# Optimization experiments

Hardware: AMD Instinct MI355X
Metric: run time of the kernel (lower is better)

Reference implementation:

```python
import jax, jax.numpy as jnp
import numpy as np

NUM_CHANNEL = 2                      # channels per telescope group
K = 7                                # hexagonal kernel size
N_LEV = [2048, 512, 128, 32, 8]      # pixels per level (stride-2 hex pooling ~ /4)
CHS = [2, 64, 128, 256, 512]         # channel progression n1->n_features->n2->n3->n4


def _iconv(x, idx, w, b):
    # x: [B,C,Nin], idx: [K,Nout], w: [O,C,K] -> [B,O,Nout]
    g = x[:, :, idx]                              # gather neighbours [B,C,K,Nout]
    return jnp.einsum('bckn,ock->bon', g, w) + b[None, :, None]


def _ipool(x, idx):
    # IndexedMaxPool2d: gather then max over kernel positions
    return x[:, :, idx].max(axis=2)               # [B,C,Nout]


def _bn(x, gamma, beta, eps=1e-5):
    # train-mode BatchNorm1d over (batch, pixel) dims, biased variance (torch semantics)
    m = x.mean(axis=(0, 2), keepdims=True)
    v = x.var(axis=(0, 2), keepdims=True)
    return (x - m) / jnp.sqrt(v + eps) * gamma[None, :, None] + beta[None, :, None]


def setup_inputs() -> dict:
    key = jax.random.key(0)
    ks = jax.random.split(key, 40)
    ki = iter(range(40))
    nk = lambda: ks[next(ki)]
    B = 256
    inp = {"x": jax.random.normal(nk(), (B, 2 * NUM_CHANNEL, N_LEV[0]), jnp.float32)}
    for i in range(4):
        inp[f"idx_conv{i+1}"] = jax.random.randint(nk(), (K, N_LEV[i]), 0, N_LEV[i])
        inp[f"idx_pool{i+1}"] = jax.random.randint(nk(), (K, N_LEV[i + 1]), 0, N_LEV[i])
        fan = float(CHS[i] * K)
        inp[f"w{i+1}"] = jax.random.normal(nk(), (CHS[i + 1], CHS[i], K), jnp.float32) / np.float32(np.sqrt(fan))
        inp[f"b{i+1}"] = jnp.zeros((CHS[i + 1],), jnp.float32)
        inp[f"gamma{i+1}"] = jnp.ones((CHS[i + 1],), jnp.float32)
        inp[f"beta{i+1}"] = jnp.zeros((CHS[i + 1],), jnp.float32)
    F = N_LEV[4] * CHS[4]            # 8 * 512 = 4096
    H = F // 2                       # 2048
    inp["lin1_w"] = jax.random.normal(nk(), (H, F), jnp.float32) / np.float32(np.sqrt(F))
    inp["lin1_b"] = jnp.zeros((H,), jnp.float32)
    inp["gamma5"] = jnp.ones((H,), jnp.float32)
    inp["beta5"] = jnp.zeros((H,), jnp.float32)
    inp["lin2_w"] = jax.random.normal(nk(), (3, H), jnp.float32) / np.float32(np.sqrt(H))
    inp["lin2_b"] = jnp.zeros((3,), jnp.float32)
    return inp


def reference(x, idx_conv1, idx_pool1, idx_conv2, idx_pool2, idx_conv3, idx_pool3,
              idx_conv4, idx_pool4, w1, b1, gamma1, beta1, w2, b2, gamma2, beta2,
              w3, b3, gamma3, beta3, w4, b4, gamma4, beta4,
              lin1_w, lin1_b, gamma5, beta5, lin2_w, lin2_b):
    layers = [(idx_conv1, idx_pool1, w1, b1, gamma1, beta1),
              (idx_conv2, idx_pool2, w2, b2, gamma2, beta2),
              (idx_conv3, idx_pool3, w3, b3, gamma3, beta3),
              (idx_conv4, idx_pool4, w4, b4, gamma4, beta4)]
    T = x.shape[1] // NUM_CHANNEL    # number of telescope groups (static)
    outs = []
    for i in range(T):
        o = x[:, i * NUM_CHANNEL:(i + 1) * NUM_CHANNEL, :]
        for (ic, ip, w, b, g, be) in layers:
            # conv -> pool -> bn -> relu (dropout with p=0 is identity)
            o = jax.nn.relu(_bn(_ipool(_iconv(o, ic, w, b), ip), g, be))
        outs.append(o)
    o = jnp.stack(outs, 1).mean(axis=1)          # [B, 512, 8]
    o = o.reshape(o.shape[0], -1)                # [B, 4096]
    o = o @ lin1_w.T + lin1_b                    # [B, 2048]
    m = o.mean(axis=0)
    v = o.var(axis=0)
    o = (o - m) / jnp.sqrt(v + 1e-5) * gamma5 + beta5
    o = jax.nn.relu(o)
    o = o @ lin2_w.T + lin2_b                    # [B, 3]
    cls = jax.nn.log_softmax(o[:, :2], axis=1)   # targets: class=2 (log-softmax), energy=1 (raw)
    return jnp.concatenate([cls, o[:, 2:3]], axis=1)
```

## Files before the change

kernel.cpp:

```cpp
#include <hip/hip_runtime.h>
#include <math.h>

#define B 256
#define KW 7

typedef __bf16 bf16x8 __attribute__((ext_vector_type(8)));
typedef __bf16 bf16x4 __attribute__((ext_vector_type(4)));
typedef float  f32x4  __attribute__((ext_vector_type(4)));

__device__ __forceinline__ void block_reduce2(float& s, float& s2, float* lds) {
    for (int off = 32; off > 0; off >>= 1) {
        s  += __shfl_down(s,  off, 64);
        s2 += __shfl_down(s2, off, 64);
    }
    int wave = threadIdx.x >> 6;
    int lane = threadIdx.x & 63;
    if (lane == 0) { lds[wave * 2] = s; lds[wave * 2 + 1] = s2; }
    __syncthreads();
    if (threadIdx.x == 0) {
        s  = lds[0] + lds[2] + lds[4] + lds[6];
        s2 = lds[1] + lds[3] + lds[5] + lds[7];
    }
}

__global__ __launch_bounds__(256) void k_transpose(const float* __restrict__ x,
                                                   float* __restrict__ A0) {
    int bid = blockIdx.x;
    int nt  = bid & 63;
    int rem = bid >> 6;
    int ci  = rem & 1;
    int t   = rem >> 1;
    int n0  = nt * 32;
    __shared__ float lds[32][257];
    int tid = threadIdx.x;
    int nl  = tid & 31;
    int bq  = tid >> 5;
    int ch  = t * 2 + ci;
    for (int p = 0; p < 32; p++) {
        int b = bq + p * 8;
        lds[nl][b] = x[((size_t)b * 4 + ch) * 2048 + n0 + nl];
    }
    __syncthreads();
    for (int nl2 = 0; nl2 < 32; nl2++) {
        A0[(((size_t)t * 2048 + n0 + nl2) * 2 + ci) * B + tid] = lds[nl2][tid];
    }
}

__global__ __launch_bounds__(256) void k_convpool1(
    const float* __restrict__ act,
    float* __restrict__ P1,
    const float* __restrict__ w,
    const float* __restrict__ bias,
    const int* __restrict__ idx_conv,
    const int* __restrict__ idx_pool,
    float* __restrict__ part1c)
{
    const int Kt = 14, C_out = 64, N_in = 2048, N_out = 512;
    int bid   = blockIdx.x;
    int cot   = bid & 1;
    int colid = bid >> 1;
    int t     = colid / N_out;
    int np    = colid - t * N_out;
    int co0   = cot << 5;

    __shared__ float lds_g[14 * 256];
    __shared__ float lds_w[14 * 33];
    __shared__ int   lds_idx[KW];

    int tid = threadIdx.x;
    int cog = tid >> 6;
    int bl  = tid & 63;

    float pmax[8][4];
    #pragma unroll
    for (int i = 0; i < 8; i++)
        #pragma unroll
        for (int j = 0; j < 4; j++) pmax[i][j] = -INFINITY;

    const float* actT = act + (size_t)t * N_in * 2 * B;

    for (int kp = 0; kp < KW; kp++) {
        int nc = idx_pool[kp * N_out + np];
        if (tid < KW) lds_idx[tid] = idx_conv[tid * N_in + nc];

        float acc[8][4];
        #pragma unroll
        for (int i = 0; i < 8; i++)
            #pragma unroll
            for (int j = 0; j < 4; j++) acc[i][j] = 0.f;

        __syncthreads();
        for (int e = tid; e < 32 * Kt; e += 256) {
            int kk = e % Kt;
            int co = e / Kt;
            lds_w[kk * 33 + co] = w[(size_t)(co0 + co) * Kt + kk];
        }
        for (int r = 0; r < Kt; r++) {
            int ci  = r / KW;
            int k   = r - ci * KW;
            int col = lds_idx[k];
            lds_g[r * 256 + tid] = actT[((size_t)col * 2 + ci) * B + tid];
        }
        __syncthreads();
        for (int kk = 0; kk < Kt; kk++) {
            float g0 = lds_g[kk * 256 + bl];
            float g1 = lds_g[kk * 256 + bl + 64];
            float g2 = lds_g[kk * 256 + bl + 128];
            float g3 = lds_g[kk * 256 + bl + 192];
            const float* wr = lds_w + kk * 33 + cog * 8;
            #pragma unroll
            for (int i = 0; i < 8; i++) {
                float wv = wr[i];
                acc[i][0] = fmaf(wv, g0, acc[i][0]);
                acc[i][1] = fmaf(wv, g1, acc[i][1]);
                acc[i][2] = fmaf(wv, g2, acc[i][2]);
                acc[i][3] = fmaf(wv, g3, acc[i][3]);
            }
        }
        #pragma unroll
        for (int i = 0; i < 8; i++)
            #pragma unroll
            for (int j = 0; j < 4; j++) pmax[i][j] = fmaxf(pmax[i][j], acc[i][j]);
    }

    float* outp = P1 + (((size_t)t * N_out + np) * C_out + co0) * B;
    float* pblk = part1c + (size_t)bid * 64;
    #pragma unroll
    for (int i = 0; i < 8; i++) {
        int co = cog * 8 + i;
        float bv = bias[co0 + co];
        float s = 0.f, s2 = 0.f;
        #pragma unroll
        for (int j = 0; j < 4; j++) {
            float val = pmax[i][j] + bv;
            outp[(size_t)co * B + bl + 64 * j] = val;
            s  += val;
            s2 += val * val;
        }
        for (int o = 32; o > 0; o >>= 1) {
            s  += __shfl_down(s,  o, 64);
            s2 += __shfl_down(s2, o, 64);
        }
        if ((tid & 63) == 0) {
            pblk[co]      = s;
            pblk[32 + co] = s2;
        }
    }
}

__global__ __launch_bounds__(256) void k_finstats1(
    const float* __restrict__ part1c,
    const float* __restrict__ gamma, const float* __restrict__ beta,
    float* __restrict__ scale, float* __restrict__ shift)
{
    int idx = blockIdx.x;
    int t = idx >> 6, c = idx & 63;
    int cot = c >> 5, cl = c & 31;
    float s = 0.f, s2 = 0.f;
    for (int np = threadIdx.x; np < 512; np += 256) {
        const float* pp = part1c + (size_t)((t * 512 + np) * 2 + cot) * 64;
        s  += pp[cl];
        s2 += pp[32 + cl];
    }
    __shared__ float lds[8];
    block_reduce2(s, s2, lds);
    if (threadIdx.x == 0) {
        float cnt  = 512.f * 256.f;
        float m    = s / cnt;
        float var  = s2 / cnt - m * m;
        float istd = rsqrtf(var + 1e-5f);
        float g    = gamma[c];
        scale[idx] = istd * g;
        shift[idx] = beta[c] - m * istd * g;
    }
}

__global__ __launch_bounds__(256) void k_bnrelu1t(
    const float* __restrict__ P1,
    const float* __restrict__ sc, const float* __restrict__ sh,
    __bf16* __restrict__ act1)
{
    int bid = blockIdx.x;
    int t = bid >> 9;
    int b = threadIdx.x;
    const float* src = P1 + (size_t)bid * 64 * B;
    __bf16* dst = act1 + (size_t)bid * B * 64 + (size_t)b * 64;
    const float* scp = sc + t * 64;
    const float* shp = sh + t * 64;
    __bf16 vals[64];
    #pragma unroll
    for (int co = 0; co < 64; co++) {
        float v = src[co * B + b];
        vals[co] = (__bf16)fmaxf(fmaf(v, scp[co], shp[co]), 0.f);
    }
    #pragma unroll
    for (int j = 0; j < 8; j++)
        *(bf16x8*)(dst + j * 8) = *(bf16x8*)&vals[j * 8];
}

__global__ __launch_bounds__(256) void k_prep(
    const float* __restrict__ w2, const float* __restrict__ w3,
    const float* __restrict__ w4, const float* __restrict__ lw1,
    __bf16* __restrict__ Wr2, __bf16* __restrict__ Wr3,
    __bf16* __restrict__ Wr4, __bf16* __restrict__ w1b)
{
    const int n2 = 128 * 448, n3 = 256 * 896, n4 = 512 * 1792, n1 = (2048 * 4096) / 8;
    int idx = blockIdx.x * 256 + threadIdx.x;
    if (idx < n2) {
        int ci = idx & 63; int r = idx >> 6; int kt = r % 7; int co = r / 7;
        Wr2[idx] = (__bf16)w2[((size_t)co * 64 + ci) * 7 + kt];
        return;
    }
    idx -= n2;
    if (idx < n3) {
        int ci = idx & 127; int r = idx >> 7; int kt = r % 7; int co = r / 7;
        Wr3[idx] = (__bf16)w3[((size_t)co * 128 + ci) * 7 + kt];
        return;
    }
    idx -= n3;
    if (idx < n4) {
        int ci = idx & 255; int r = idx >> 8; int kt = r % 7; int co = r / 7;
        Wr4[idx] = (__bf16)w4[((size_t)co * 256 + ci) * 7 + kt];
        return;
    }
    idx -= n4;
    if (idx < n1) {
        const f32x4* s4 = (const f32x4*)(lw1 + (size_t)idx * 8);
        f32x4 a = s4[0], b = s4[1];
        bf16x8 v;
        v[0] = (__bf16)a[0]; v[1] = (__bf16)a[1]; v[2] = (__bf16)a[2]; v[3] = (__bf16)a[3];
        v[4] = (__bf16)b[0]; v[5] = (__bf16)b[1]; v[6] = (__bf16)b[2]; v[7] = (__bf16)b[3];
        *(bf16x8*)(w1b + (size_t)idx * 8) = v;
    }
}

__global__ __launch_bounds__(256) void k_conv_mfma(
    const __bf16* __restrict__ act,
    __bf16* __restrict__ convo,
    const __bf16* __restrict__ wr,
    const int* __restrict__ idx_conv,
    int C_in, int C_out, int N, int ci_shift)
{
    int nco = C_out >> 7;
    int bid = blockIdx.x;
    int cot = bid % nco;
    int rem = bid / nco;
    int n   = rem % N;
    int t   = rem / N;
    int co0 = cot * 128;
    int Kt  = C_in * KW;

    int tid  = threadIdx.x;
    int wv   = tid >> 6;
    int lane = tid & 63;
    int quad = lane >> 4;
    int lid  = lane & 15;

    int cols[KW];
    #pragma unroll
    for (int k = 0; k < KW; k++) cols[k] = idx_conv[k * N + n];

    f32x4 acc[8][4];
    #pragma unroll
    for (int i = 0; i < 8; i++)
        #pragma unroll
        for (int j = 0; j < 4; j++) {
            acc[i][j][0] = 0.f; acc[i][j][1] = 0.f;
            acc[i][j][2] = 0.f; acc[i][j][3] = 0.f;
        }

    const __bf16* actT  = act + (size_t)t * N * B * C_in
                              + ((size_t)(wv * 64 + lid)) * C_in + quad * 8;
    const __bf16* wbase = wr + (size_t)(co0 + lid) * Kt + quad * 8;

    int niter = Kt >> 5;

    bf16x8 bcur[4], bnxt[4];
    {
        const __bf16* g = actT + (size_t)cols[0] * B * C_in;
        #pragma unroll
        for (int bt = 0; bt < 4; bt++)
            bcur[bt] = *(const bf16x8*)(g + (size_t)bt * 16 * C_in);
    }

    for (int it = 0; it < niter; it++) {
        int k0 = it << 5;
        if (it + 1 < niter) {
            int k1  = k0 + 32;
            int kt  = k1 >> ci_shift;
            int ci0 = k1 & (C_in - 1);
            const __bf16* g = actT + (size_t)cols[kt] * B * C_in + ci0;
            #pragma unroll
            for (int bt = 0; bt < 4; bt++)
                bnxt[bt] = *(const bf16x8*)(g + (size_t)bt * 16 * C_in);
        }
        #pragma unroll
        for (int rt = 0; rt < 8; rt++) {
            bf16x8 afrag = *(const bf16x8*)(wbase + (size_t)rt * 16 * Kt + k0);
            #pragma unroll
            for (int bt = 0; bt < 4; bt++)
                acc[rt][bt] = __builtin_amdgcn_mfma_f32_16x16x32_bf16(
                    afrag, bcur[bt], acc[rt][bt], 0, 0, 0);
        }
        #pragma unroll
        for (int bt = 0; bt < 4; bt++) bcur[bt] = bnxt[bt];
    }

    __bf16* outp = convo + ((size_t)(t * N + n) * B) * C_out;
    #pragma unroll
    for (int rt = 0; rt < 8; rt++)
        #pragma unroll
        for (int bt = 0; bt < 4; bt++) {
            int b  = wv * 64 + bt * 16 + lid;
            int co = co0 + rt * 16 + quad * 4;
            bf16x4 v;
            v[0] = (__bf16)acc[rt][bt][0];
            v[1] = (__bf16)acc[rt][bt][1];
            v[2] = (__bf16)acc[rt][bt][2];
            v[3] = (__bf16)acc[rt][bt][3];
            *(bf16x4*)(outp + (size_t)b * C_out + co) = v;
        }
}

__global__ __launch_bounds__(256) void k_poolstats(
    const __bf16* __restrict__ convo,
    float* __restrict__ P,
    const float* __restrict__ bias,
    const int* __restrict__ idx_pool,
    float* __restrict__ part,
    int C, int N, int No)
{
    int bid  = blockIdx.x;
    int bg   = bid & 3;
    int rem  = bid >> 2;
    int np   = rem % No;
    int t    = rem / No;
    int cols[7];
    #pragma unroll
    for (int k = 0; k < 7; k++) cols[k] = idx_pool[k * No + np];
    const __bf16* base = convo + (size_t)t * N * B * C;
    float* pout = P + ((size_t)(t * No + np) * B) * C;
    int tid = threadIdx.x;
    float s[2] = {0.f, 0.f}, s2[2] = {0.f, 0.f};
    int NC, c0, bstart, bstep, nb;
    if (C >= 256) { NC = C >> 8; c0 = tid;           bstart = 0;        bstep = 1; nb = 64; }
    else          { NC = 1;      c0 = tid & (C - 1); bstart = tid >> 7; bstep = 2; nb = 32; }
    for (int j = 0; j < NC; j++) {
        int c = c0 + j * 256;
        float bv = bias[c];
        for (int i = 0; i < nb; i++) {
            int b = bg * 64 + bstart + i * bstep;
            float m = -1e30f;
            #pragma unroll
            for (int k = 0; k < 7; k++) {
                float v = (float)base[((size_t)cols[k] * B + b) * C + c];
                m = fmaxf(m, v);
            }
            float val = m + bv;
            pout[(size_t)b * C + c] = val;
            s[j] += val; s2[j] += val * val;
        }
    }
    float* pp = part + (size_t)((t * No + np) * 4 + bg) * 1024;
    for (int j = 0; j < NC; j++) {
        pp[tid + j * 256]       = s[j];
        pp[512 + tid + j * 256] = s2[j];
    }
}

__global__ __launch_bounds__(256) void k_finstats(
    const float* __restrict__ part,
    const float* __restrict__ gamma, const float* __restrict__ beta,
    float* __restrict__ scale, float* __restrict__ shift,
    int C, int No)
{
    int idx = blockIdx.x;
    int t = idx / C, c = idx - t * C;
    int SMAX   = C < 256 ? 256 : C;
    int nslice = SMAX / C;
    int nblk   = No * 4;
    int total  = nblk * nslice;
    const float* pbase = part + (size_t)(t * No * 4) * 1024;
    float s = 0.f, s2 = 0.f;
    for (int e = threadIdx.x; e < total; e += 256) {
        int blk = e / nslice;
        int j   = e - blk * nslice;
        const float* pp = pbase + (size_t)blk * 1024;
        int sl = c + j * C;
        s  += pp[sl];
        s2 += pp[512 + sl];
    }
    __shared__ float lds[8];
    block_reduce2(s, s2, lds);
    if (threadIdx.x == 0) {
        float cnt  = (float)No * 256.f;
        float m    = s / cnt;
        float var  = s2 / cnt - m * m;
        float istd = rsqrtf(var + 1e-5f);
        float g    = gamma[c];
        scale[idx] = istd * g;
        shift[idx] = beta[c] - m * istd * g;
    }
}

__global__ void k_bnrelu(const float* __restrict__ P, __bf16* __restrict__ act,
                         const float* __restrict__ scale, const float* __restrict__ shift,
                         int C, int total)
{
    int idx = blockIdx.x * 256 + threadIdx.x;
    if (idx >= total) return;
    int c = idx & (C - 1);
    int t = idx >= (total >> 1) ? 1 : 0;
    int tc = t * C + c;
    float v = P[idx];
    act[idx] = (__bf16)fmaxf(fmaf(v, scale[tc], shift[tc]), 0.f);
}

__global__ __launch_bounds__(256) void k_zbuild(const float* __restrict__ P4,
                                                const float* __restrict__ sc4,
                                                const float* __restrict__ sh4,
                                                __bf16* __restrict__ z)
{
    int b = blockIdx.x;
    int tid = threadIdx.x;
    for (int j = 0; j < 2; j++) {
        int c = tid + j * 256;
        float s0 = sc4[c],       h0 = sh4[c];
        float s1 = sc4[512 + c], h1 = sh4[512 + c];
        #pragma unroll
        for (int np = 0; np < 8; np++) {
            float v0 = P4[(((size_t)0 * 8 + np) * B + b) * 512 + c];
            float v1 = P4[(((size_t)1 * 8 + np) * B + b) * 512 + c];
            float y0 = fmaxf(fmaf(v0, s0, h0), 0.f);
            float y1 = fmaxf(fmaf(v1, s1, h1), 0.f);
            z[(size_t)b * 4096 + c * 8 + np] = (__bf16)(0.5f * (y0 + y1));
        }
    }
}

__global__ __launch_bounds__(256) void k_lin1_part(
    const __bf16* __restrict__ zb,
    const __bf16* __restrict__ w1b,
    float* __restrict__ partL)
{
    int ht = blockIdx.x >> 3;
    int ks = blockIdx.x & 7;
    int h0 = ht * 64;
    int f_beg = ks * 512, f_end = f_beg + 512;

    int tid  = threadIdx.x;
    int wv   = tid >> 6;
    int lane = tid & 63;
    int quad = lane >> 4;
    int lid  = lane & 15;

    f32x4 acc[4][4];
    #pragma unroll
    for (int i = 0; i < 4; i++)
        #pragma unroll
        for (int j = 0; j < 4; j++) {
            acc[i][j][0] = 0.f; acc[i][j][1] = 0.f;
            acc[i][j][2] = 0.f; acc[i][j][3] = 0.f;
        }

    const __bf16* wbase = w1b + (size_t)(h0 + lid) * 4096 + quad * 8;
    const __bf16* zbase = zb + ((size_t)(wv * 64 + lid)) * 4096 + quad * 8;

    for (int f0 = f_beg; f0 < f_end; f0 += 32) {
        bf16x8 afrag[4];
        #pragma unroll
        for (int rt = 0; rt < 4; rt++)
            afrag[rt] = *(const bf16x8*)(wbase + (size_t)rt * 16 * 4096 + f0);
        bf16x8 bfrag[4];
        #pragma unroll
        for (int bt = 0; bt < 4; bt++)
            bfrag[bt] = *(const bf16x8*)(zbase + (size_t)bt * 16 * 4096 + f0);
        #pragma unroll
        for (int rt = 0; rt < 4; rt++)
            #pragma unroll
            for (int bt = 0; bt < 4; bt++)
                acc[rt][bt] = __builtin_amdgcn_mfma_f32_16x16x32_bf16(
                    afrag[rt], bfrag[bt], acc[rt][bt], 0, 0, 0);
    }
    float* outp = partL + (size_t)ks * 2048 * B;
    #pragma unroll
    for (int rt = 0; rt < 4; rt++)
        #pragma unroll
        for (int bt = 0; bt < 4; bt++) {
            int b = wv * 64 + bt * 16 + lid;
            int h = h0 + rt * 16 + quad * 4;
            #pragma unroll
            for (int r = 0; r < 4; r++)
                outp[(size_t)(h + r) * B + b] = acc[rt][bt][r];
        }
}

__global__ __launch_bounds__(256) void k_redstats5(
    const float* __restrict__ partL,
    const float* __restrict__ b1,
    const float* __restrict__ gamma5, const float* __restrict__ beta5,
    float* __restrict__ o1,
    float* __restrict__ scale5, float* __restrict__ shift5)
{
    int h = blockIdx.x;
    int b = threadIdx.x;
    float v = b1[h];
    #pragma unroll
    for (int s = 0; s < 8; s++)
        v += partL[((size_t)s * 2048 + h) * B + b];
    o1[(size_t)h * B + b] = v;
    float s1 = v, s2 = v * v;
    __shared__ float lds[8];
    block_reduce2(s1, s2, lds);
    if (threadIdx.x == 0) {
        float m    = s1 * (1.f / 256.f);
        float var  = s2 * (1.f / 256.f) - m * m;
        float istd = rsqrtf(var + 1e-5f);
        float g    = gamma5[h];
        scale5[h]  = istd * g;
        shift5[h]  = beta5[h] - m * istd * g;
    }
}

__global__ __launch_bounds__(256) void k_final(
    const float* __restrict__ o1,
    const float* __restrict__ scale5, const float* __restrict__ shift5,
    const float* __restrict__ w2, const float* __restrict__ b2,
    float* __restrict__ out)
{
    int b = blockIdx.x;
    int tid = threadIdx.x;
    float s0 = 0.f, s1 = 0.f, s2v = 0.f;
    for (int h = tid; h < 2048; h += 256) {
        float y = fmaxf(fmaf(o1[(size_t)h * B + b], scale5[h], shift5[h]), 0.f);
        s0  = fmaf(y, w2[h],        s0);
        s1  = fmaf(y, w2[2048 + h], s1);
        s2v = fmaf(y, w2[4096 + h], s2v);
    }
    for (int off = 32; off > 0; off >>= 1) {
        s0  += __shfl_down(s0,  off, 64);
        s1  += __shfl_down(s1,  off, 64);
        s2v += __shfl_down(s2v, off, 64);
    }
    __shared__ float lds[12];
    int wave = tid >> 6, lane = tid & 63;
    if (lane == 0) { lds[wave * 3] = s0; lds[wave * 3 + 1] = s1; lds[wave * 3 + 2] = s2v; }
    __syncthreads();
    if (tid == 0) {
        float o0 = lds[0] + lds[3] + lds[6] + lds[9]  + b2[0];
        float oa = lds[1] + lds[4] + lds[7] + lds[10] + b2[1];
        float ob = lds[2] + lds[5] + lds[8] + lds[11] + b2[2];
        float m   = fmaxf(o0, oa);
        float lse = m + logf(expf(o0 - m) + expf(oa - m));
        out[b * 3 + 0] = o0 - lse;
        out[b * 3 + 1] = oa - lse;
        out[b * 3 + 2] = ob;
    }
}

extern "C" void kernel_launch(void* const* d_in, const int* in_sizes, int n_in,
                              void* d_out, int out_size, void* d_ws, size_t ws_size,
                              hipStream_t stream) {
    (void)in_sizes; (void)n_in; (void)out_size; (void)ws_size;

    const float* x   = (const float*)d_in[0];
    const int*   ic1 = (const int*)d_in[1];
    const int*   ip1 = (const int*)d_in[2];
    const float* pW1 = (const float*)d_in[3];
    const float* pB1 = (const float*)d_in[4];
    const float* pG1 = (const float*)d_in[5];
    const float* pE1 = (const float*)d_in[6];
    const int*   ic2 = (const int*)d_in[7];
    const int*   ip2 = (const int*)d_in[8];
    const float* pW2 = (const float*)d_in[9];
    const float* pB2 = (const float*)d_in[10];
    const float* pG2 = (const float*)d_in[11];
    const float* pE2 = (const float*)d_in[12];
    const int*   ic3 = (const int*)d_in[13];
    const int*   ip3 = (const int*)d_in[14];
    const float* pW3 = (const float*)d_in[15];
    const float* pB3 = (const float*)d_in[16];
    const float* pG3 = (const float*)d_in[17];
    const float* pE3 = (const float*)d_in[18];
    const int*   ic4 = (const int*)d_in[19];
    const int*   ip4 = (const int*)d_in[20];
    const float* pW4 = (const float*)d_in[21];
    const float* pB4 = (const float*)d_in[22];
    const float* pG4 = (const float*)d_in[23];
    const float* pE4 = (const float*)d_in[24];
    const float* lw1 = (const float*)d_in[25];
    const float* lb1 = (const float*)d_in[26];
    const float* g5  = (const float*)d_in[27];
    const float* e5  = (const float*)d_in[28];
    const float* lw2 = (const float*)d_in[29];
    const float* lb2 = (const float*)d_in[30];

    char* ws = (char*)d_ws;
    size_t off = 0;
    auto alloc = [&](size_t bytes) -> char* {
        char* p = ws + off;
        off += (bytes + 511) & ~(size_t)511;
        return p;
    };

    float*  A0    = (float*) alloc((size_t)2 * 2048 * 2 * B * 4);
    __bf16* act1  = (__bf16*)alloc((size_t)2 * 512 * B * 64 * 2);
    char*   U     =          alloc((size_t)512 * B * 128 * 4);
    float*  P1f   = (float*)U;
    __bf16* convX = (__bf16*)U;
    float*  partL = (float*)U;
    float*  Pf    = (float*) alloc((size_t)2 * 128 * B * 128 * 4);
    __bf16* actS  = (__bf16*)alloc((size_t)2 * 128 * B * 128 * 2);
    __bf16* Wr2   = (__bf16*)alloc((size_t)128 * 448 * 2);
    __bf16* Wr3   = (__bf16*)alloc((size_t)256 * 896 * 2);
    __bf16* Wr4   = (__bf16*)alloc((size_t)512 * 1792 * 2);
    __bf16* w1b   = (__bf16*)alloc((size_t)2048 * 4096 * 2);
    __bf16* z     = (__bf16*)alloc((size_t)256 * 4096 * 2);
    float*  o1    = (float*) alloc((size_t)2048 * B * 4);
    float*  part  = (float*) alloc((size_t)2 * 128 * 4 * 1024 * 4);
    float*  part1c= (float*) alloc((size_t)2048 * 64 * 4);
    float*  sc1 = (float*)alloc(2 * 64 * 4);
    float*  sh1 = (float*)alloc(2 * 64 * 4);
    float*  sc2 = (float*)alloc(2 * 128 * 4);
    float*  sh2 = (float*)alloc(2 * 128 * 4);
    float*  sc3 = (float*)alloc(2 * 256 * 4);
    float*  sh3 = (float*)alloc(2 * 256 * 4);
    float*  sc4 = (float*)alloc(2 * 512 * 4);
    float*  sh4 = (float*)alloc(2 * 512 * 4);
    float*  sc5 = (float*)alloc(2048 * 4);
    float*  sh5 = (float*)alloc(2048 * 4);

    {
        const int total = 128 * 448 + 256 * 896 + 512 * 1792 + (2048 * 4096) / 8;
        k_prep<<<(total + 255) / 256, 256, 0, stream>>>(pW2, pW3, pW4, lw1,
                                                        Wr2, Wr3, Wr4, w1b);
    }

    k_transpose<<<256, 256, 0, stream>>>(x, A0);

    k_convpool1<<<2048, 256, 0, stream>>>(A0, P1f, pW1, pB1, ic1, ip1, part1c);
    k_finstats1<<<2 * 64, 256, 0, stream>>>(part1c, pG1, pE1, sc1, sh1);
    k_bnrelu1t<<<2 * 512, 256, 0, stream>>>(P1f, sc1, sh1, act1);

    k_conv_mfma<<<1 * 512 * 2, 256, 0, stream>>>(act1, convX, Wr2, ic2, 64, 128, 512, 6);
    k_poolstats<<<2 * 128 * 4, 256, 0, stream>>>(convX, Pf, pB2, ip2, part, 128, 512, 128);
    k_finstats<<<2 * 128, 256, 0, stream>>>(part, pG2, pE2, sc2, sh2, 128, 128);
    k_bnrelu<<<(2 * 128 * B * 128) / 256, 256, 0, stream>>>(Pf, actS, sc2, sh2, 128, 2 * 128 * B * 128);

    k_conv_mfma<<<2 * 128 * 2, 256, 0, stream>>>(actS, convX, Wr3, ic3, 128, 256, 128, 7);
    k_poolstats<<<2 * 32 * 4, 256, 0, stream>>>(convX, Pf, pB3, ip3, part, 256, 128, 32);
    k_finstats<<<2 * 256, 256, 0, stream>>>(part, pG3, pE3, sc3, sh3, 256, 32);
    k_bnrelu<<<(2 * 32 * B * 256) / 256, 256, 0, stream>>>(Pf, actS, sc3, sh3, 256, 2 * 32 * B * 256);

    k_conv_mfma<<<4 * 32 * 2, 256, 0, stream>>>(actS, convX, Wr4, ic4, 256, 512, 32, 8);
    k_poolstats<<<2 * 8 * 4, 256, 0, stream>>>(convX, Pf, pB4, ip4, part, 512, 32, 8);
    k_finstats<<<2 * 512, 256, 0, stream>>>(part, pG4, pE4, sc4, sh4, 512, 8);

    k_zbuild<<<256, 256, 0, stream>>>(Pf, sc4, sh4, z);
    k_lin1_part<<<256, 256, 0, stream>>>(z, w1b, partL);
    k_redstats5<<<2048, 256, 0, stream>>>(partL, lb1, g5, e5, o1, sc5, sh5);
    k_final<<<256, 256, 0, stream>>>(o1, sc5, sh5, lw2, lb2, (float*)d_out);
}
```

Measured before the change: 713.5 us.

## Stage conv weight panels in LDS and deepen activation prefetch to two iterations

The MFMA conv kernel now cooperatively loads 128x224 weight panels into shared memory, padded to a stride of 232, once per panel. Previously each of the four waves read the same weight fragments from global memory on its own, and the staging is meant to remove that redundant global and L2 traffic. Activation gathers are now prefetched two iterations ahead instead of one to hide more load latency. The cost is two block barriers per panel, about 58 KB of LDS per block, and extra registers, all of which may lower occupancy. The panel loop assumes Kt is a multiple of 224 (C_in a multiple of 32).

```diff
diff --git a/kernel.cpp b/kernel.cpp
--- a/kernel.cpp
+++ b/kernel.cpp
@@ -7,6 +7,9 @@
 typedef __bf16 bf16x8 __attribute__((ext_vector_type(8)));
 typedef __bf16 bf16x4 __attribute__((ext_vector_type(4)));
 typedef float  f32x4  __attribute__((ext_vector_type(4)));
+
+#define KPAN 224
+#define PSTR 232
 
 __device__ __forceinline__ void block_reduce2(float& s, float& s2, float* lds) {
     for (int off = 32; off > 0; off >>= 1) {
@@ -250,6 +253,8 @@
     int co0 = cot * 128;
     int Kt  = C_in * KW;
 
+    __shared__ __bf16 lds_w[128 * PSTR];
+
     int tid  = threadIdx.x;
     int wv   = tid >> 6;
     int lane = tid & 63;
@@ -269,41 +274,54 @@
             acc[i][j][2] = 0.f; acc[i][j][3] = 0.f;
         }
 
-    const __bf16* actT  = act + (size_t)t * N * B * C_in
-                              + ((size_t)(wv * 64 + lid)) * C_in + quad * 8;
-    const __bf16* wbase = wr + (size_t)(co0 + lid) * Kt + quad * 8;
+    const __bf16* actT = act + (size_t)t * N * B * C_in
+                             + ((size_t)(wv * 64 + lid)) * C_in + quad * 8;
 
     int niter = Kt >> 5;
-
-    bf16x8 bcur[4], bnxt[4];
-    {
-        const __bf16* g = actT + (size_t)cols[0] * B * C_in;
+    int npan  = Kt / KPAN;
+
+    bf16x8 bcur[4], bn1[4], bn2[4];
+
+    auto loadB = [&](int it, bf16x8* dst) {
+        int k   = it << 5;
+        int kt  = k >> ci_shift;
+        int ci0 = k & (C_in - 1);
+        const __bf16* g = actT + (size_t)cols[kt] * B * C_in + ci0;
         #pragma unroll
         for (int bt = 0; bt < 4; bt++)
-            bcur[bt] = *(const bf16x8*)(g + (size_t)bt * 16 * C_in);
-    }
-
-    for (int it = 0; it < niter; it++) {
-        int k0 = it << 5;
-        if (it + 1 < niter) {
-            int k1  = k0 + 32;
-            int kt  = k1 >> ci_shift;
-            int ci0 = k1 & (C_in - 1);
-            const __bf16* g = actT + (size_t)cols[kt] * B * C_in + ci0;
-            #pragma unroll
-            for (int bt = 0; bt < 4; bt++)
-                bnxt[bt] = *(const bf16x8*)(g + (size_t)bt * 16 * C_in);
-        }
-        #pragma unroll
-        for (int rt = 0; rt < 8; rt++) {
-            bf16x8 afrag = *(const bf16x8*)(wbase + (size_t)rt * 16 * Kt + k0);
-            #pragma unroll
-            for (int bt = 0; bt < 4; bt++)
-                acc[rt][bt] = __builtin_amdgcn_mfma_f32_16x16x32_bf16(
-                    afrag, bcur[bt], acc[rt][bt], 0, 0, 0);
-        }
-        #pragma unroll
-        for (int bt = 0; bt < 4; bt++) bcur[bt] = bnxt[bt];
+            dst[bt] = *(const bf16x8*)(g + (size_t)bt * 16 * C_in);
+    };
+
+    loadB(0, bcur);
+    loadB(1, bn1);
+
+    for (int p = 0; p < npan; p++) {
+        int kp0 = p * KPAN;
+        __syncthreads();
+        #pragma unroll
+        for (int i = 0; i < 14; i++) {
+            int seg = tid + 256 * i;
+            int row = seg / 28;
+            int c8  = seg - row * 28;
+            *(bf16x8*)&lds_w[row * PSTR + c8 * 8] =
+                *(const bf16x8*)(wr + (size_t)(co0 + row) * Kt + kp0 + c8 * 8);
+        }
+        __syncthreads();
+        #pragma unroll
+        for (int kk = 0; kk < 7; kk++) {
+            int it = p * 7 + kk;
+            if (it + 2 < niter) loadB(it + 2, bn2);
+            #pragma unroll
+            for (int rt = 0; rt < 8; rt++) {
+                bf16x8 afrag = *(const bf16x8*)&lds_w[(rt * 16 + lid) * PSTR + kk * 32 + quad * 8];
+                #pragma unroll
+                for (int bt = 0; bt < 4; bt++)
+                    acc[rt][bt] = __builtin_amdgcn_mfma_f32_16x16x32_bf16(
+                        afrag, bcur[bt], acc[rt][bt], 0, 0, 0);
+            }
+            #pragma unroll
+            for (int bt = 0; bt < 4; bt++) { bcur[bt] = bn1[bt]; bn1[bt] = bn2[bt]; }
+        }
     }
 
     __bf16* outp = convo + ((size_t)(t * N + n) * B) * C_out;
```

Measured after the change: 659.0 us. 7.6% less time.
